# Optimization experiments

Hardware: AMD Instinct MI355X
Metric: run time of the kernel (lower is better)

The kernel has to match this reference:

```python
import jax, jax.numpy as jnp
import numpy as np

N, E, IN, H, O, ED = 20000, 100000, 167, 4, 256, 10
HID = H * O  # 1024
BN_EPS = 1e-5


def _bn(x, g, b):
    # BatchNorm1d in training mode: batch statistics over nodes
    mu = x.mean(0)
    var = x.var(0)
    return (x - mu) * jax.lax.rsqrt(var + BN_EPS) * g + b


def _gat(x, src, dst, ef, Wg, We, attn, at, cb, heads, out):
    # modified_GAT: multi-head attention with edge features + time scalar
    n = x.shape[0]
    h = (x @ Wg).reshape(n, heads, out)                 # [N,H,O]
    e = (ef[:, 1:] @ We).reshape(-1, heads, out)        # [E,H,O] edge-feature proj
    t = ef[:, 0]                                        # [E] time feature
    # node-level attention scores (avoids materializing [E,H,O] twice)
    s_src = jnp.einsum('nhd,hd->nh', h, attn[0])
    s_dst = jnp.einsum('nhd,hd->nh', h, attn[1])
    s_e = jnp.einsum('ehd,hd->eh', e, attn[2])
    logits = jax.nn.leaky_relu(s_src[src] + s_dst[dst] + s_e + t[:, None] * at, 0.2)  # [E,H]
    # attention normalization: softmax over incoming edges of each dst node
    m = jax.ops.segment_max(logits, dst, num_segments=n)
    m = jnp.where(jnp.isfinite(m), m, 0.0)
    p = jnp.exp(logits - m[dst])
    denom = jax.ops.segment_sum(p, dst, num_segments=n)
    w = p / (denom[dst] + 1e-16)                        # [E,H]
    msg = w[:, :, None] * (h[src] + e)                  # [E,H,O]
    agg = jax.ops.segment_sum(msg, dst, num_segments=n) # [N,H,O]
    return agg.reshape(n, heads * out) + cb


def setup_inputs() -> dict:
    key = jax.random.key(0)
    ks = iter(jax.random.split(key, 64))

    def nrm(shape, s):
        return jax.random.normal(next(ks), shape, dtype=jnp.float32) * np.float32(s)

    d = {}
    d['x'] = jax.random.normal(next(ks), (N, IN), dtype=jnp.float32)
    d['edge_index'] = jax.random.randint(next(ks), (2, E), 0, N)
    d['edge_attr'] = jax.random.uniform(next(ks), (E, ED + 2), dtype=jnp.float32)
    conv_dims = [(IN, H, O), (HID, H, O), (HID, 1, 2)]
    for i, (fin, hh, oo) in enumerate(conv_dims, 1):
        d[f'Wg{i}'] = nrm((fin, hh * oo), 1.0 / np.sqrt(fin))
        d[f'We{i}'] = nrm((ED, hh * oo), 1.0 / np.sqrt(ED))
        d[f'attn{i}'] = nrm((3, hh, oo), 0.1)
        d[f'at{i}'] = nrm((hh,), 0.1)
        d[f'cb{i}'] = jnp.zeros((hh * oo,), jnp.float32)
    lin_dims = [(IN, HID), (HID, HID), (HID, 2)]
    bn_dims = [IN, HID, HID]
    for i, (fin, fo) in enumerate(lin_dims, 1):
        d[f'lw{i}'] = nrm((fin, fo), 1.0 / np.sqrt(fin))
        d[f'lb{i}'] = jnp.zeros((fo,), jnp.float32)
        d[f'g{i}'] = jnp.ones((bn_dims[i - 1],), jnp.float32)
        d[f'b{i}'] = jnp.zeros((bn_dims[i - 1],), jnp.float32)
    return d


def reference(x, edge_index, edge_attr,
              Wg1, We1, attn1, at1, cb1, lw1, lb1, g1, b1,
              Wg2, We2, attn2, at2, cb2, lw2, lb2, g2, b2,
              Wg3, We3, attn3, at3, cb3, lw3, lb3, g3, b3):
    src, dst = edge_index[0], edge_index[1]
    ef = edge_attr[:, :-1]  # drop edge class column
    h = _bn(x, g1, b1)
    h = jax.nn.relu(h @ lw1 + lb1 + _gat(h, src, dst, ef, Wg1, We1, attn1, at1, cb1, H, O))
    h = _bn(h, g2, b2)
    h = jax.nn.relu(h @ lw2 + lb2 + _gat(h, src, dst, ef, Wg2, We2, attn2, at2, cb2, H, O))
    h = _bn(h, g3, b3)
    h = jax.nn.relu(h @ lw3 + lb3 + _gat(h, src, dst, ef, Wg3, We3, attn3, at3, cb3, 1, 2))
    return h
```

## Files before the change

kernel.cpp:

```cpp
#include <hip/hip_runtime.h>
#include <math.h>

#define NN 20000
#define EE 100000
#define FIN 167
#define KP1 256
#define HID 1024
#define OO 256
#define NB 16

typedef unsigned short u16;
typedef short bf16x8 __attribute__((ext_vector_type(8)));
typedef short s16x4  __attribute__((ext_vector_type(4)));
typedef float f32x4  __attribute__((ext_vector_type(4)));

__device__ __forceinline__ float bf(u16 u){ return __uint_as_float(((unsigned)u)<<16); }
__device__ __forceinline__ u16 fb(float v){
  unsigned u = __float_as_uint(v);
  return (u16)((u + 0x7FFFu + ((u>>16)&1u)) >> 16);
}
__device__ __forceinline__ float ldv(const float* p, long i){ return p[i]; }
__device__ __forceinline__ float ldv(const u16*   p, long i){ return bf(p[i]); }

__global__ void k_count(const int* __restrict__ ei, int* __restrict__ counts){
  int e = blockIdx.x*256 + threadIdx.x;
  if (e < EE) atomicAdd(&counts[ei[EE+e]], 1);
}

__global__ __launch_bounds__(256) void k_scan(const int* __restrict__ counts, int* __restrict__ iptr){
  __shared__ int sd[256];
  int tid = threadIdx.x;
  int carry = 0;
  for (int base=0; base<NN; base+=256){
    int i = base+tid;
    int v = (i<NN)? counts[i] : 0;
    sd[tid]=v;
    __syncthreads();
    for (int off=1; off<256; off<<=1){
      int t = (tid>=off)? sd[tid-off] : 0;
      __syncthreads();
      sd[tid] += t;
      __syncthreads();
    }
    if (i<NN) iptr[i] = carry + sd[tid] - v;
    carry += sd[255];
    __syncthreads();
  }
  if (tid==0) iptr[NN]=carry;
}

__global__ void k_fill(const int* __restrict__ ei, const int* __restrict__ iptr,
                       int* __restrict__ cursor, int* __restrict__ eid){
  int e = blockIdx.x*256 + threadIdx.x;
  if (e < EE){
    int d = ei[EE+e];
    int pos = atomicAdd(&cursor[d],1);
    eid[iptr[d]+pos] = e;
  }
}

template<typename T>
__global__ void k_bnstats(const T* __restrict__ X, float* __restrict__ sums, int F){
  int f = blockIdx.y*256 + threadIdx.x;
  if (f >= F) return;
  int r0 = blockIdx.x*100, r1 = r0+100;
  float s=0.f, s2=0.f;
  for (int r=r0;r<r1;r++){ float v = ldv(X,(long)r*F+f); s += v; s2 += v*v; }
  atomicAdd(&sums[f], s);
  atomicAdd(&sums[F+f], s2);
}

__global__ void k_bnfin(const float* __restrict__ sums, const float* __restrict__ g,
                        const float* __restrict__ b, float* __restrict__ scale,
                        float* __restrict__ shift, int F){
  int f = blockIdx.x*256 + threadIdx.x;
  if (f >= F) return;
  float mu  = sums[f]   * (1.f/NN);
  float var = sums[F+f] * (1.f/NN) - mu*mu;
  float sc  = rsqrtf(var + 1e-5f) * g[f];
  scale[f] = sc;
  shift[f] = b[f] - mu*sc;
}

__global__ __launch_bounds__(256) void k_foldT(const float* __restrict__ Wg, const float* __restrict__ Wl,
                        const float* __restrict__ scale,
                        u16* __restrict__ Wt, int K, int Kp){
  __shared__ float t[32][33];
  int k0 = blockIdx.x*32, c0 = blockIdx.y*32;
  int tx = threadIdx.x & 31, ty = threadIdx.x >> 5;
  bool second = (c0 >= HID);
  const float* W = second ? Wl : Wg;
  int cc0 = second ? c0 - HID : c0;
  #pragma unroll
  for (int i=0;i<4;i++){
    int k = k0 + ty + i*8;
    t[ty+i*8][tx] = (k < K) ? W[(long)k*HID + cc0 + tx] * scale[k] : 0.f;
  }
  __syncthreads();
  #pragma unroll
  for (int i=0;i<4;i++){
    int c = c0 + ty + i*8;
    Wt[(long)c*Kp + k0 + tx] = fb(t[tx][ty+i*8]);
  }
}

__global__ void k_cinit(const float* __restrict__ lb, float* __restrict__ cst){
  int c = blockIdx.x*256 + threadIdx.x;
  if (c < 2*HID) cst[c] = (c >= HID) ? lb[c-HID] : 0.f;
}

__global__ __launch_bounds__(256) void k_const(const float* __restrict__ Wg, const float* __restrict__ Wl,
                        const float* __restrict__ shift, float* __restrict__ cst, int K){
  int tx = threadIdx.x & 63, ty = threadIdx.x >> 6;
  int c = blockIdx.x*64 + tx;
  bool second = c >= HID;
  const float* W = second ? Wl : Wg;
  int cc = second ? c-HID : c;
  int k0 = blockIdx.y*128;
  int k1 = min(K, k0+128);
  float s = 0.f;
  for (int k=k0+ty; k<k1; k+=4) s += shift[k]*W[(long)k*HID+cc];
  __shared__ float red[256];
  red[threadIdx.x] = s;
  __syncthreads();
  if (ty == 0){
    float tot = red[tx] + red[tx+64] + red[tx+128] + red[tx+192];
    atomicAdd(&cst[c], tot);
  }
}

__global__ void k_cast(const float* __restrict__ x, u16* __restrict__ xb){
  long idx = (long)blockIdx.x*256 + threadIdx.x;
  if (idx >= (long)NN*KP1) return;
  int n = (int)(idx / KP1), k = (int)(idx % KP1);
  xb[idx] = (k<FIN)? fb(x[(long)n*FIN+k]) : (u16)0;
}

__global__ void k_we16(const float* __restrict__ We, u16* __restrict__ We16){
  int i = blockIdx.x*256 + threadIdx.x;
  if (i < 10*HID) We16[i] = fb(We[i]);
}

#define MF(a_,b_,c_) __builtin_amdgcn_mfma_f32_16x16x32_bf16(a_,b_,c_,0,0,0)
#define FENCE asm volatile("" ::: "memory")
#define BAR do { FENCE; __builtin_amdgcn_s_barrier(); FENCE; } while(0)

__global__ __launch_bounds__(512,2) void k_gemm(const u16* __restrict__ A, int K,
                     const u16* __restrict__ Wt, const float* __restrict__ cst,
                     u16* __restrict__ Chg, u16* __restrict__ Clin){
  __shared__ u16 lds[2][24576];
  int b = blockIdx.x;
  int wg = (b & 7)*158 + (b >> 3);
  int row0 = (wg >> 4)*256, col0 = (wg & 15)*128;
  int tid = threadIdx.x;
  int wave = tid >> 6, lane = tid & 63, quad = lane >> 4, lo = lane & 15;
  int wm = wave >> 1, wn = wave & 1;
  const u16* Apt[2];
  #pragma unroll
  for (int i=0;i<2;i++){
    int s = i*512 + tid, srow = s>>2;
    int gr = row0 + srow; if (gr >= NN) gr = NN-1;
    Apt[i] = A + (long)gr*K + (((s&3)^(srow&3))*8);
  }
  int brow = tid>>2;
  const u16* Bpt = Wt + (long)(col0 + brow)*K + ((((tid&3)^(brow&3)))*8);
  const char* ldsc = (const char*)&lds[0][0];
  int axor = lo & 3;
  int aoff = (wm*64 + lo)*64 + ((quad^axor)*16);
  int boff = 32768 + (wn*64 + lo)*64 + ((quad^axor)*16);
  int NT = K >> 6;
  f32x4 acc[4][4] = {};
  {
    u16* d = (u16*)&lds[0][0];
    __builtin_amdgcn_global_load_lds(Apt[0],      d +          tid*8, 16, 0, 0);
    __builtin_amdgcn_global_load_lds(Apt[1],      d +  4096 +  tid*8, 16, 0, 0);
    __builtin_amdgcn_global_load_lds(Bpt,         d + 16384 +  tid*8, 16, 0, 0);
    __builtin_amdgcn_global_load_lds(Apt[0] + 32, d +  8192 +  tid*8, 16, 0, 0);
    __builtin_amdgcn_global_load_lds(Apt[1] + 32, d + 12288 +  tid*8, 16, 0, 0);
    __builtin_amdgcn_global_load_lds(Bpt    + 32, d + 20480 +  tid*8, 16, 0, 0);
    asm volatile("s_waitcnt vmcnt(3)" ::: "memory");
    BAR;
  }
  for (int t=0; t<NT; t++){
    const char* Lb = ldsc + (t&1)*49152;
    u16* Sb = (u16*)&lds[0][0] + ((t&1)^1)*24576;
    int k0n = (t+1) << 6;
    int nx = (t+1 < NT);
    bf16x8 af[4], bfr[4];
    #pragma unroll
    for (int i=0;i<4;i++) af[i]  = *(const bf16x8*)(Lb + aoff + i*1024);
    #pragma unroll
    for (int n=0;n<4;n++) bfr[n] = *(const bf16x8*)(Lb + boff + n*1024);
    if (nx){
      __builtin_amdgcn_global_load_lds(Apt[0] + k0n, Sb +          tid*8, 16, 0, 0);
      __builtin_amdgcn_global_load_lds(Apt[1] + k0n, Sb +  4096 +  tid*8, 16, 0, 0);
      __builtin_amdgcn_global_load_lds(Bpt    + k0n, Sb + 16384 +  tid*8, 16, 0, 0);
    }
    #pragma unroll
    for (int i=0;i<4;i++)
      #pragma unroll
      for (int n=0;n<4;n++)
        acc[i][n] = MF(af[i], bfr[n], acc[i][n]);
    if (nx) asm volatile("s_waitcnt vmcnt(3)" ::: "memory");
    else    asm volatile("s_waitcnt vmcnt(0)" ::: "memory");
    BAR;
    #pragma unroll
    for (int i=0;i<4;i++) af[i]  = *(const bf16x8*)(Lb + 16384 + aoff + i*1024);
    #pragma unroll
    for (int n=0;n<4;n++) bfr[n] = *(const bf16x8*)(Lb +  8192 + boff + n*1024);
    if (nx){
      __builtin_amdgcn_global_load_lds(Apt[0] + k0n + 32, Sb +  8192 +  tid*8, 16, 0, 0);
      __builtin_amdgcn_global_load_lds(Apt[1] + k0n + 32, Sb + 12288 +  tid*8, 16, 0, 0);
      __builtin_amdgcn_global_load_lds(Bpt    + k0n + 32, Sb + 20480 +  tid*8, 16, 0, 0);
    }
    #pragma unroll
    for (int i=0;i<4;i++)
      #pragma unroll
      for (int n=0;n<4;n++)
        acc[i][n] = MF(af[i], bfr[n], acc[i][n]);
    if (nx) asm volatile("s_waitcnt vmcnt(3)" ::: "memory");
    BAR;
  }
  #pragma unroll
  for (int i=0;i<4;i++){
    #pragma unroll
    for (int n=0;n<4;n++){
      int col = col0 + wn*64 + n*16 + lo;
      float cs = cst[col];
      #pragma unroll
      for (int r=0;r<4;r++){
        int row = row0 + wm*64 + i*16 + quad*4 + r;
        if (row < NN){
          u16 o = fb(acc[i][n][r] + cs);
          if (col < HID) Chg[(long)row*HID + col] = o;
          else           Clin[(long)row*HID + col - HID] = o;
        }
      }
    }
  }
}
#undef MF
#undef BAR
#undef FENCE

__global__ __launch_bounds__(256) void k_sdot(const u16* __restrict__ hg, const float* __restrict__ attn,
                       float* __restrict__ ssrc, float* __restrict__ sdst){
  int unit = blockIdx.x*4 + (threadIdx.x >> 6);
  if (unit >= NN*4) return;
  int lane = threadIdx.x & 63;
  int n = unit >> 2, h = unit & 3;
  const u16* hp = hg + (long)n*HID + h*OO + lane*4;
  s16x4 v = *(const s16x4*)hp;
  float4 x0 = *(const float4*)(attn + h*OO + lane*4);
  float4 x1 = *(const float4*)(attn + HID + h*OO + lane*4);
  float f0 = bf((u16)v.x), f1 = bf((u16)v.y), f2 = bf((u16)v.z), f3 = bf((u16)v.w);
  float ss = f0*x0.x + f1*x0.y + f2*x0.z + f3*x0.w;
  float sd = f0*x1.x + f1*x1.y + f2*x1.z + f3*x1.w;
  #pragma unroll
  for (int off=32; off>0; off>>=1){
    ss += __shfl_down(ss, off);
    sd += __shfl_down(sd, off);
  }
  if (lane==0){ ssrc[unit]=ss; sdst[unit]=sd; }
}

__global__ void k_q(const float* __restrict__ We, const float* __restrict__ attn,
                    float* __restrict__ q){
  int t = threadIdx.x;
  if (t >= 40) return;
  int k = t >> 2, h = t & 3;
  float s = 0.f;
  for (int d=0; d<OO; d++) s += We[(long)k*HID + h*OO + d] * attn[2*HID + h*OO + d];
  q[k*4+h] = s;
}

__global__ void k_logits(const int* __restrict__ ei, const float* __restrict__ ea,
                         const float* __restrict__ q, const float* __restrict__ at,
                         const float* __restrict__ ssrc, const float* __restrict__ sdst,
                         float* __restrict__ L){
  int idx = blockIdx.x*256 + threadIdx.x;
  if (idx >= EE*4) return;
  int e = idx >> 2, h = idx & 3;
  int s = ei[e], dd = ei[EE+e];
  float se = 0.f;
  #pragma unroll
  for (int k=0;k<10;k++) se += ea[e*12+1+k] * q[k*4+h];
  float v = ssrc[s*4+h] + sdst[dd*4+h] + se + ea[e*12]*at[h];
  L[idx] = (v>0.f)? v : 0.2f*v;
}

__global__ void k_mden(const int* __restrict__ iptr, const int* __restrict__ eid,
                       const float* __restrict__ ea, float* __restrict__ L,
                       float* __restrict__ cw){
  int idx = blockIdx.x*256 + threadIdx.x;
  if (idx >= NN*4) return;
  int n = idx >> 2, h = idx & 3;
  int b = iptr[n], e1 = iptr[n+1];
  float mx = -INFINITY;
  for (int i=b;i<e1;i++) mx = fmaxf(mx, L[eid[i]*4+h]);
  if (b == e1) mx = 0.f;
  float s = 0.f;
  for (int i=b;i<e1;i++) s += expf(L[eid[i]*4+h] - mx);
  float dv = 1.f/(s + 1e-16f);
  float c[10] = {0.f,0.f,0.f,0.f,0.f,0.f,0.f,0.f,0.f,0.f};
  for (int i=b;i<e1;i++){
    int e = eid[i];
    float w = expf(L[e*4+h]-mx)*dv;
    L[e*4+h] = w;
    #pragma unroll
    for (int k=0;k<10;k++) c[k] += w*ea[e*12+1+k];
  }
  float* cp = cw + (long)idx*10;
  #pragma unroll
  for (int k=0;k<10;k++) cp[k] = c[k];
}

__global__ __launch_bounds__(256) void k_gath(
    const u16* __restrict__ hg, const int* __restrict__ ei,
    const int* __restrict__ iptr, const int* __restrict__ eid,
    const float* __restrict__ L,
    const float* __restrict__ cw,
    const u16* __restrict__ We16, const float* __restrict__ cb,
    u16* __restrict__ lio)
{
  __shared__ u16  sWe[10*HID];
  __shared__ float scb[HID];
  int tid = threadIdx.x;
  for (int i=tid;i<10*HID;i+=256) sWe[i] = We16[i];
  for (int i=tid;i<HID;i+=256) scb[i] = cb[i];
  __syncthreads();
  int d0 = blockIdx.x*NB, dend = min(NN, d0+NB);
  for (int d=d0; d<dend; d++){
    float acc[4];
    #pragma unroll
    for (int j=0;j<4;j++) acc[j] = bf(lio[(long)d*HID + tid + j*256]);
    int b0 = iptr[d], en = iptr[d+1];
    for (int i=b0;i<en;i++){
      int e = eid[i], s_ = ei[e];
      float4 w4 = *(const float4*)(L + (long)e*4);
      const u16* hgs = hg + (long)s_*HID + tid;
      acc[0] += w4.x*bf(hgs[0]);
      acc[1] += w4.y*bf(hgs[256]);
      acc[2] += w4.z*bf(hgs[512]);
      acc[3] += w4.w*bf(hgs[768]);
    }
    const float* cp = cw + (long)d*40;
    #pragma unroll
    for (int j=0;j<4;j++){
      float ew = 0.f;
      #pragma unroll
      for (int k=0;k<10;k++) ew += cp[j*10+k]*bf(sWe[k*HID + tid + j*256]);
      acc[j] += ew;
    }
    #pragma unroll
    for (int j=0;j<4;j++){
      int f = tid + j*256;
      lio[(long)d*HID+f] = fb(fmaxf(acc[j] + scb[f], 0.f));
    }
  }
}

__global__ __launch_bounds__(256) void k_n3(
    const u16* __restrict__ in, const float* __restrict__ scale, const float* __restrict__ shift,
    const float* __restrict__ Wg, const float* __restrict__ lw, const float* __restrict__ lb,
    const float* __restrict__ attn,
    float* __restrict__ hg3, float* __restrict__ lin3,
    float* __restrict__ ssrc, float* __restrict__ sdst)
{
  __shared__ float xin[1024];
  __shared__ float red[256];
  int n = blockIdx.x, tid = threadIdx.x;
  for (int k=tid;k<HID;k+=256) xin[k] = bf(in[(long)n*HID+k])*scale[k]+shift[k];
  __syncthreads();
  float p[4] = {0.f,0.f,0.f,0.f};
  for (int k=tid;k<HID;k+=256){
    float xv = xin[k];
    p[0] += xv*Wg[k*2];   p[1] += xv*Wg[k*2+1];
    p[2] += xv*lw[k*2];   p[3] += xv*lw[k*2+1];
  }
  float r[4];
  for (int q=0;q<4;q++){
    red[tid]=p[q]; __syncthreads();
    for (int o=128;o>0;o>>=1){ if(tid<o) red[tid]+=red[tid+o]; __syncthreads(); }
    r[q]=red[0]; __syncthreads();
  }
  if (tid==0){
    hg3[n*2]   = r[0];
    hg3[n*2+1] = r[1];
    lin3[n*2]   = r[2] + lb[0];
    lin3[n*2+1] = r[3] + lb[1];
    ssrc[n] = r[0]*attn[0] + r[1]*attn[1];
    sdst[n] = r[0]*attn[2] + r[1]*attn[3];
  }
}

__global__ void k_logits3(const int* __restrict__ ei, const float* __restrict__ ea,
                          const float* __restrict__ We, const float* __restrict__ attn,
                          const float* __restrict__ at, const float* __restrict__ ssrc,
                          const float* __restrict__ sdst, float* __restrict__ L){
  int e = blockIdx.x*256 + threadIdx.x;
  if (e >= EE) return;
  int s = ei[e], d = ei[EE+e];
  float e0=0.f, e1=0.f;
  #pragma unroll
  for (int k=0;k<10;k++){
    float c = ea[e*12+1+k];
    e0 += c*We[k*2]; e1 += c*We[k*2+1];
  }
  float se = e0*attn[4] + e1*attn[5];
  float v = ssrc[s] + sdst[d] + se + ea[e*12]*at[0];
  L[e] = (v>0.f)? v : 0.2f*v;
}

__global__ void k_mden3(const int* __restrict__ iptr, const int* __restrict__ eid,
                        const float* __restrict__ ea, float* __restrict__ L,
                        float* __restrict__ cw){
  int n = blockIdx.x*256 + threadIdx.x;
  if (n >= NN) return;
  int b = iptr[n], e1 = iptr[n+1];
  float mx = -INFINITY;
  for (int i=b;i<e1;i++) mx = fmaxf(mx, L[eid[i]]);
  if (b == e1) mx = 0.f;
  float s = 0.f;
  for (int i=b;i<e1;i++) s += expf(L[eid[i]] - mx);
  float dv = 1.f/(s+1e-16f);
  float c[10] = {0.f,0.f,0.f,0.f,0.f,0.f,0.f,0.f,0.f,0.f};
  for (int i=b;i<e1;i++){
    int e = eid[i];
    float w = expf(L[e]-mx)*dv;
    L[e] = w;
    #pragma unroll
    for (int k=0;k<10;k++) c[k] += w*ea[e*12+1+k];
  }
  float* cp = cw + (long)n*10;
  #pragma unroll
  for (int k=0;k<10;k++) cp[k] = c[k];
}

__global__ void k_gather3(const int* __restrict__ ei,
                          const int* __restrict__ iptr, const int* __restrict__ eid,
                          const float* __restrict__ L,
                          const float* __restrict__ cw,
                          const float* __restrict__ hg3,
                          const float* __restrict__ We, const float* __restrict__ lin3,
                          const float* __restrict__ cb, float* __restrict__ out){
  int n = blockIdx.x*256 + threadIdx.x;
  if (n >= NN) return;
  int b = iptr[n], en = iptr[n+1];
  const float* cp = cw + (long)n*10;
  float e0f=0.f, e1f=0.f;
  #pragma unroll
  for (int k=0;k<10;k++){ e0f += cp[k]*We[k*2]; e1f += cp[k]*We[k*2+1]; }
  float a0=0.f, a1=0.f;
  for (int i=b;i<en;i++){
    int e = eid[i], s_ = ei[e];
    float w = L[e];
    a0 += w*hg3[s_*2];
    a1 += w*hg3[s_*2+1];
  }
  out[n*2]   = fmaxf(lin3[n*2]  +a0+e0f+cb[0], 0.f);
  out[n*2+1] = fmaxf(lin3[n*2+1]+a1+e1f+cb[1], 0.f);
}

extern "C" void kernel_launch(void* const* d_in, const int* in_sizes, int n_in,
                              void* d_out, int out_size, void* d_ws, size_t ws_size,
                              hipStream_t stream){
  const int* ei = (const int*)d_in[1];

  long long sz[64];
  {
    const long long* s64 = (const long long*)(const void*)in_sizes;
    bool is64 = (n_in >= 2) && (in_sizes[0] == 3340000) && (in_sizes[1] == 0)
                && (s64[1] == 200000);
    for (int i=0;i<n_in && i<64;i++) sz[i] = is64 ? s64[i] : (long long)in_sizes[i];
  }

  int IWg[3], IWe[3], IAttn[3], IAt[3], ICb[3], ILw[3], ILb[3], IG[3], IB[3];
  if (n_in > 8 && sz[8] == (long long)HID*HID){
    for (int l=0;l<3;l++){
      IWg[l]=3+l*5; IWe[l]=4+l*5; IAttn[l]=5+l*5; IAt[l]=6+l*5; ICb[l]=7+l*5;
      ILw[l]=18+l*4; ILb[l]=19+l*4; IG[l]=20+l*4; IB[l]=21+l*4;
    }
  } else {
    int idx=3;
    for (int l=0;l<3;l++){
      IWg[l]=idx++; IWe[l]=idx++; IAttn[l]=idx++; IAt[l]=idx++; ICb[l]=idx++;
      ILw[l]=idx++; ILb[l]=idx++; IG[l]=idx++; IB[l]=idx++;
    }
  }
  #define FP(i) ((const float*)d_in[(i)])

  char* ws = (char*)d_ws;
  size_t off = 0;
  auto alloc = [&](size_t bytes)->void*{ void* p = ws + off; off += (bytes + 255) & ~(size_t)255; return p; };
  auto G = [](long n){ return (int)((n+255)/256); };

  u16*   buf0 = (u16*)  alloc((size_t)NN*HID*2);
  u16*   bufA = (u16*)  alloc((size_t)NN*HID*2);
  u16*   bufB = (u16*)  alloc((size_t)NN*HID*2);
  u16*   xbf  = (u16*)  alloc((size_t)NN*KP1*2);
  u16*   Wt   = (u16*)  alloc((size_t)2*HID*HID*2);
  u16*   We16 = (u16*)  alloc((size_t)10*HID*2);
  float* cst  = (float*)alloc(2*HID*4);
  float* L    = (float*)alloc((size_t)EE*4*4);
  float* m    = (float*)alloc((size_t)NN*4*4);
  float* dinv = (float*)alloc((size_t)NN*4*4);
  float* ssrc = (float*)alloc((size_t)NN*4*4);
  float* sdst = (float*)alloc((size_t)NN*4*4);
  int*   iptr = (int*)  alloc((size_t)(NN+4)*4);
  int*   cnts = (int*)  alloc((size_t)NN*4);
  int*   eid  = (int*)  alloc((size_t)EE*4);
  float* stats= (float*)alloc(2*HID*4);
  float* scale= (float*)alloc(HID*4);
  float* shift= (float*)alloc(HID*4);
  float* qbuf = (float*)alloc(64*4);
  float* hg3  = (float*)alloc((size_t)NN*2*4);
  float* lin3 = (float*)alloc((size_t)NN*2*4);
  float* cw   = (float*)alloc((size_t)NN*40*4);

  hipMemsetAsync(cnts, 0, NN*sizeof(int), stream);
  k_count<<<G(EE),256,0,stream>>>(ei, cnts);
  k_scan<<<1,256,0,stream>>>(cnts, iptr);
  hipMemsetAsync(cnts, 0, NN*sizeof(int), stream);
  k_fill<<<G(EE),256,0,stream>>>(ei, iptr, cnts, eid);

  int gg = 1264;
  int gsd = (NN*4+3)/4;

  {
    hipMemsetAsync(stats, 0, 2*FIN*sizeof(float), stream);
    dim3 bg(200, 1);
    k_bnstats<float><<<bg,256,0,stream>>>(FP(0), stats, FIN);
    k_bnfin<<<1,256,0,stream>>>(stats, FP(IG[0]), FP(IB[0]), scale, shift, FIN);
    k_cast<<<G((long)NN*KP1),256,0,stream>>>(FP(0), xbf);
    dim3 ft(KP1/32, 64);
    k_foldT<<<ft,256,0,stream>>>(FP(IWg[0]), FP(ILw[0]), scale, Wt, FIN, KP1);
    k_cinit<<<8,256,0,stream>>>(FP(ILb[0]), cst);
    dim3 cg(32, (FIN+127)/128);
    k_const<<<cg,256,0,stream>>>(FP(IWg[0]), FP(ILw[0]), shift, cst, FIN);
    k_we16<<<40,256,0,stream>>>(FP(IWe[0]), We16);
    k_gemm<<<gg,512,0,stream>>>(xbf, KP1, Wt, cst, buf0, bufA);
    k_sdot<<<gsd,256,0,stream>>>(buf0, FP(IAttn[0]), ssrc, sdst);
    k_q<<<1,64,0,stream>>>(FP(IWe[0]), FP(IAttn[0]), qbuf);
    k_logits<<<G(EE*4),256,0,stream>>>(ei, FP(2), qbuf, FP(IAt[0]), ssrc, sdst, L);
    k_mden<<<G(NN*4),256,0,stream>>>(iptr, eid, FP(2), L, cw);
    k_gath<<<(NN+NB-1)/NB,256,0,stream>>>(buf0, ei, iptr, eid, L, cw,
                                          We16, FP(ICb[0]), bufA);
  }
  {
    hipMemsetAsync(stats, 0, 2*HID*sizeof(float), stream);
    dim3 bg(200, 4);
    k_bnstats<u16><<<bg,256,0,stream>>>(bufA, stats, HID);
    k_bnfin<<<4,256,0,stream>>>(stats, FP(IG[1]), FP(IB[1]), scale, shift, HID);
    dim3 ft(HID/32, 64);
    k_foldT<<<ft,256,0,stream>>>(FP(IWg[1]), FP(ILw[1]), scale, Wt, HID, HID);
    k_cinit<<<8,256,0,stream>>>(FP(ILb[1]), cst);
    dim3 cg(32, HID/128);
    k_const<<<cg,256,0,stream>>>(FP(IWg[1]), FP(ILw[1]), shift, cst, HID);
    k_we16<<<40,256,0,stream>>>(FP(IWe[1]), We16);
    k_gemm<<<gg,512,0,stream>>>(bufA, HID, Wt, cst, buf0, bufB);
    k_sdot<<<gsd,256,0,stream>>>(buf0, FP(IAttn[1]), ssrc, sdst);
    k_q<<<1,64,0,stream>>>(FP(IWe[1]), FP(IAttn[1]), qbuf);
    k_logits<<<G(EE*4),256,0,stream>>>(ei, FP(2), qbuf, FP(IAt[1]), ssrc, sdst, L);
    k_mden<<<G(NN*4),256,0,stream>>>(iptr, eid, FP(2), L, cw);
    k_gath<<<(NN+NB-1)/NB,256,0,stream>>>(buf0, ei, iptr, eid, L, cw,
                                          We16, FP(ICb[1]), bufB);
  }

  hipMemsetAsync(stats, 0, 2*HID*sizeof(float), stream);
  dim3 bg3(200, 4);
  k_bnstats<u16><<<bg3,256,0,stream>>>(bufB, stats, HID);
  k_bnfin<<<4,256,0,stream>>>(stats, FP(IG[2]), FP(IB[2]), scale, shift, HID);
  k_n3<<<NN,256,0,stream>>>(bufB, scale, shift, FP(IWg[2]), FP(ILw[2]), FP(ILb[2]),
                            FP(IAttn[2]), hg3, lin3, ssrc, sdst);
  k_logits3<<<G(EE),256,0,stream>>>(ei, FP(2), FP(IWe[2]), FP(IAttn[2]), FP(IAt[2]), ssrc, sdst, L);
  k_mden3<<<G(NN),256,0,stream>>>(iptr, eid, FP(2), L, cw);
  k_gather3<<<G(NN),256,0,stream>>>(ei, iptr, eid, L, cw, hg3,
                                    FP(IWe[2]), lin3, FP(ICb[2]), (float*)d_out);
}
```

Measured before the change: 912.5 us.

## Vectorize BN stats, logits, softmax kernels and fold BN into layer-3 projection

Several memory-bound kernels are reworked. BN statistics now read 8 bf16 values per thread with a shared-memory reduction and far fewer atomics. Logits and the per-node softmax now handle all 4 heads per thread using float4 loads, so each edge's attributes and indices are loaded once. The layer-3 node projection folds the BN scale and shift into a small precomputed weight and constant, then processes 4 nodes per block with wavefront shuffle reductions instead of one node per block with repeated tree reductions. The cost is fewer threads in the softmax kernel (one per node) and more registers per thread for the 40 accumulators.

```diff
diff --git a/kernel.cpp b/kernel.cpp
--- a/kernel.cpp
+++ b/kernel.cpp
@@ -68,6 +68,34 @@
   for (int r=r0;r<r1;r++){ float v = ldv(X,(long)r*F+f); s += v; s2 += v*v; }
   atomicAdd(&sums[f], s);
   atomicAdd(&sums[F+f], s2);
+}
+
+__global__ __launch_bounds__(256) void k_bnstats8(const u16* __restrict__ X, float* __restrict__ sums){
+  int tid = threadIdx.x;
+  int f8 = (tid & 127)*8;
+  int rbase = blockIdx.x*500;
+  float s[8]={0,0,0,0,0,0,0,0}, s2[8]={0,0,0,0,0,0,0,0};
+  for (int r=rbase + (tid>>7); r<rbase+500; r+=2){
+    bf16x8 v = *(const bf16x8*)(X + (long)r*HID + f8);
+    #pragma unroll
+    for (int j=0;j<8;j++){ float x=bf((u16)v[j]); s[j]+=x; s2[j]+=x*x; }
+  }
+  __shared__ float red[256][8];
+  #pragma unroll
+  for (int j=0;j<8;j++) red[tid][j]=s[j];
+  __syncthreads();
+  if (tid<128){
+    #pragma unroll
+    for (int j=0;j<8;j++) atomicAdd(&sums[f8+j], red[tid][j]+red[tid+128][j]);
+  }
+  __syncthreads();
+  #pragma unroll
+  for (int j=0;j<8;j++) red[tid][j]=s2[j];
+  __syncthreads();
+  if (tid<128){
+    #pragma unroll
+    for (int j=0;j<8;j++) atomicAdd(&sums[HID+f8+j], red[tid][j]+red[tid+128][j]);
+  }
 }
 
 __global__ void k_bnfin(const float* __restrict__ sums, const float* __restrict__ g,
@@ -278,41 +306,68 @@
                          const float* __restrict__ q, const float* __restrict__ at,
                          const float* __restrict__ ssrc, const float* __restrict__ sdst,
                          float* __restrict__ L){
-  int idx = blockIdx.x*256 + threadIdx.x;
-  if (idx >= EE*4) return;
-  int e = idx >> 2, h = idx & 3;
+  int e = blockIdx.x*256 + threadIdx.x;
+  if (e >= EE) return;
   int s = ei[e], dd = ei[EE+e];
-  float se = 0.f;
-  #pragma unroll
-  for (int k=0;k<10;k++) se += ea[e*12+1+k] * q[k*4+h];
-  float v = ssrc[s*4+h] + sdst[dd*4+h] + se + ea[e*12]*at[h];
-  L[idx] = (v>0.f)? v : 0.2f*v;
+  float4 a0 = *(const float4*)(ea + (long)e*12);
+  float4 a1 = *(const float4*)(ea + (long)e*12 + 4);
+  float4 a2 = *(const float4*)(ea + (long)e*12 + 8);
+  float t = a0.x;
+  float cc[10] = {a0.y,a0.z,a0.w, a1.x,a1.y,a1.z,a1.w, a2.x,a2.y,a2.z};
+  float4 ss = *(const float4*)(ssrc + (long)s*4);
+  float4 sd = *(const float4*)(sdst + (long)dd*4);
+  float sv[4] = {ss.x+sd.x, ss.y+sd.y, ss.z+sd.z, ss.w+sd.w};
+  float4 out;
+  #pragma unroll
+  for (int h=0;h<4;h++){
+    float se = 0.f;
+    #pragma unroll
+    for (int k=0;k<10;k++) se += cc[k]*q[k*4+h];
+    float v = sv[h] + se + t*at[h];
+    ((float*)&out)[h] = (v>0.f)? v : 0.2f*v;
+  }
+  *(float4*)(L + (long)e*4) = out;
 }
 
 __global__ void k_mden(const int* __restrict__ iptr, const int* __restrict__ eid,
                        const float* __restrict__ ea, float* __restrict__ L,
                        float* __restrict__ cw){
-  int idx = blockIdx.x*256 + threadIdx.x;
-  if (idx >= NN*4) return;
-  int n = idx >> 2, h = idx & 3;
+  int n = blockIdx.x*256 + threadIdx.x;
+  if (n >= NN) return;
   int b = iptr[n], e1 = iptr[n+1];
-  float mx = -INFINITY;
-  for (int i=b;i<e1;i++) mx = fmaxf(mx, L[eid[i]*4+h]);
-  if (b == e1) mx = 0.f;
-  float s = 0.f;
-  for (int i=b;i<e1;i++) s += expf(L[eid[i]*4+h] - mx);
-  float dv = 1.f/(s + 1e-16f);
-  float c[10] = {0.f,0.f,0.f,0.f,0.f,0.f,0.f,0.f,0.f,0.f};
+  float m0=-INFINITY, m1=-INFINITY, m2=-INFINITY, m3=-INFINITY;
+  for (int i=b;i<e1;i++){
+    float4 l = *(const float4*)(L + (long)eid[i]*4);
+    m0=fmaxf(m0,l.x); m1=fmaxf(m1,l.y); m2=fmaxf(m2,l.z); m3=fmaxf(m3,l.w);
+  }
+  if (b==e1){ m0=m1=m2=m3=0.f; }
+  float s0=0.f,s1=0.f,s2=0.f,s3=0.f;
+  for (int i=b;i<e1;i++){
+    float4 l = *(const float4*)(L + (long)eid[i]*4);
+    s0+=expf(l.x-m0); s1+=expf(l.y-m1); s2+=expf(l.z-m2); s3+=expf(l.w-m3);
+  }
+  float d0=1.f/(s0+1e-16f), d1=1.f/(s1+1e-16f), d2=1.f/(s2+1e-16f), d3=1.f/(s3+1e-16f);
+  float c[4][10] = {};
   for (int i=b;i<e1;i++){
     int e = eid[i];
-    float w = expf(L[e*4+h]-mx)*dv;
-    L[e*4+h] = w;
-    #pragma unroll
-    for (int k=0;k<10;k++) c[k] += w*ea[e*12+1+k];
-  }
-  float* cp = cw + (long)idx*10;
-  #pragma unroll
-  for (int k=0;k<10;k++) cp[k] = c[k];
+    float4 l = *(const float4*)(L + (long)e*4);
+    float4 w = { expf(l.x-m0)*d0, expf(l.y-m1)*d1, expf(l.z-m2)*d2, expf(l.w-m3)*d3 };
+    *(float4*)(L + (long)e*4) = w;
+    float4 a0 = *(const float4*)(ea + (long)e*12);
+    float4 a1 = *(const float4*)(ea + (long)e*12 + 4);
+    float4 a2 = *(const float4*)(ea + (long)e*12 + 8);
+    float cc[10] = {a0.y,a0.z,a0.w, a1.x,a1.y,a1.z,a1.w, a2.x,a2.y,a2.z};
+    #pragma unroll
+    for (int k=0;k<10;k++){
+      c[0][k] += w.x*cc[k]; c[1][k] += w.y*cc[k];
+      c[2][k] += w.z*cc[k]; c[3][k] += w.w*cc[k];
+    }
+  }
+  float* cp = cw + (long)n*40;
+  #pragma unroll
+  for (int h=0;h<4;h++)
+    #pragma unroll
+    for (int k=0;k<10;k++) cp[h*10+k] = c[h][k];
 }
 
 __global__ __launch_bounds__(256) void k_gath(
@@ -360,37 +415,76 @@
   }
 }
 
-__global__ __launch_bounds__(256) void k_n3(
-    const u16* __restrict__ in, const float* __restrict__ scale, const float* __restrict__ shift,
-    const float* __restrict__ Wg, const float* __restrict__ lw, const float* __restrict__ lb,
+__global__ void k_c4init(const float* __restrict__ lb, float* __restrict__ c4){
+  if (threadIdx.x==0 && blockIdx.x==0){ c4[0]=0.f; c4[1]=0.f; c4[2]=lb[0]; c4[3]=lb[1]; }
+}
+
+__global__ __launch_bounds__(256) void k_fold3(const float* __restrict__ Wg, const float* __restrict__ lw,
+                        const float* __restrict__ scale, const float* __restrict__ shift,
+                        float* __restrict__ W4, float* __restrict__ c4){
+  int k = blockIdx.x*256 + threadIdx.x;
+  float sc = scale[k], sh = shift[k];
+  float w0=Wg[k*2], w1=Wg[k*2+1], l0=lw[k*2], l1=lw[k*2+1];
+  float4 o = {w0*sc, w1*sc, l0*sc, l1*sc};
+  *(float4*)(W4 + (long)k*4) = o;
+  __shared__ float red[256][4];
+  int tid = threadIdx.x;
+  red[tid][0]=sh*w0; red[tid][1]=sh*w1; red[tid][2]=sh*l0; red[tid][3]=sh*l1;
+  __syncthreads();
+  for (int o2=128;o2>0;o2>>=1){
+    if (tid<o2){
+      #pragma unroll
+      for (int j=0;j<4;j++) red[tid][j]+=red[tid+o2][j];
+    }
+    __syncthreads();
+  }
+  if (tid==0){
+    #pragma unroll
+    for (int j=0;j<4;j++) atomicAdd(&c4[j], red[0][j]);
+  }
+}
+
+__global__ __launch_bounds__(256) void k_n3(const u16* __restrict__ in,
+    const float* __restrict__ W4, const float* __restrict__ c4,
     const float* __restrict__ attn,
     float* __restrict__ hg3, float* __restrict__ lin3,
     float* __restrict__ ssrc, float* __restrict__ sdst)
 {
-  __shared__ float xin[1024];
-  __shared__ float red[256];
-  int n = blockIdx.x, tid = threadIdx.x;
-  for (int k=tid;k<HID;k+=256) xin[k] = bf(in[(long)n*HID+k])*scale[k]+shift[k];
-  __syncthreads();
-  float p[4] = {0.f,0.f,0.f,0.f};
-  for (int k=tid;k<HID;k+=256){
-    float xv = xin[k];
-    p[0] += xv*Wg[k*2];   p[1] += xv*Wg[k*2+1];
-    p[2] += xv*lw[k*2];   p[3] += xv*lw[k*2+1];
-  }
-  float r[4];
-  for (int q=0;q<4;q++){
-    red[tid]=p[q]; __syncthreads();
-    for (int o=128;o>0;o>>=1){ if(tid<o) red[tid]+=red[tid+o]; __syncthreads(); }
-    r[q]=red[0]; __syncthreads();
-  }
-  if (tid==0){
-    hg3[n*2]   = r[0];
-    hg3[n*2+1] = r[1];
-    lin3[n*2]   = r[2] + lb[0];
-    lin3[n*2+1] = r[3] + lb[1];
-    ssrc[n] = r[0]*attn[0] + r[1]*attn[1];
-    sdst[n] = r[0]*attn[2] + r[1]*attn[3];
+  __shared__ float sW[HID*4];
+  __shared__ float sx[4][HID];
+  int tid = threadIdx.x;
+  int n0 = blockIdx.x*4;
+  for (int i=tid; i<HID; i+=256) *(float4*)&sW[i*4] = *(const float4*)(W4 + (long)i*4);
+  for (int idx=tid; idx<512; idx+=256){
+    int rr = idx>>7, ch = idx&127;
+    bf16x8 v = *(const bf16x8*)(in + (long)(n0+rr)*HID + ch*8);
+    #pragma unroll
+    for (int j=0;j<8;j++) sx[rr][ch*8+j] = bf((u16)v[j]);
+  }
+  __syncthreads();
+  int w = tid>>6, lane = tid&63;
+  float p0=0.f,p1=0.f,p2=0.f,p3=0.f;
+  #pragma unroll
+  for (int g=0; g<16; g++){
+    int k = g*64 + lane;
+    float x = sx[w][k];
+    float4 wv = *(const float4*)&sW[k*4];
+    p0 += x*wv.x; p1 += x*wv.y; p2 += x*wv.z; p3 += x*wv.w;
+  }
+  #pragma unroll
+  for (int off=32; off>0; off>>=1){
+    p0 += __shfl_down(p0, off);
+    p1 += __shfl_down(p1, off);
+    p2 += __shfl_down(p2, off);
+    p3 += __shfl_down(p3, off);
+  }
+  if (lane==0){
+    int n = n0 + w;
+    float r0=p0+c4[0], r1=p1+c4[1], r2=p2+c4[2], r3=p3+c4[3];
+    hg3[n*2]=r0; hg3[n*2+1]=r1;
+    lin3[n*2]=r2; lin3[n*2+1]=r3;
+    ssrc[n]=r0*attn[0]+r1*attn[1];
+    sdst[n]=r0*attn[2]+r1*attn[3];
   }
 }
 
@@ -503,8 +597,6 @@
   u16*   We16 = (u16*)  alloc((size_t)10*HID*2);
   float* cst  = (float*)alloc(2*HID*4);
   float* L    = (float*)alloc((size_t)EE*4*4);
-  float* m    = (float*)alloc((size_t)NN*4*4);
-  float* dinv = (float*)alloc((size_t)NN*4*4);
   float* ssrc = (float*)alloc((size_t)NN*4*4);
   float* sdst = (float*)alloc((size_t)NN*4*4);
   int*   iptr = (int*)  alloc((size_t)(NN+4)*4);
@@ -517,6 +609,8 @@
   float* hg3  = (float*)alloc((size_t)NN*2*4);
   float* lin3 = (float*)alloc((size_t)NN*2*4);
   float* cw   = (float*)alloc((size_t)NN*40*4);
+  float* W4   = (float*)alloc((size_t)HID*4*4);
+  float* c4   = (float*)alloc(4*4);
 
   hipMemsetAsync(cnts, 0, NN*sizeof(int), stream);
   k_count<<<G(EE),256,0,stream>>>(ei, cnts);
@@ -542,15 +636,14 @@
     k_gemm<<<gg,512,0,stream>>>(xbf, KP1, Wt, cst, buf0, bufA);
     k_sdot<<<gsd,256,0,stream>>>(buf0, FP(IAttn[0]), ssrc, sdst);
     k_q<<<1,64,0,stream>>>(FP(IWe[0]), FP(IAttn[0]), qbuf);
-    k_logits<<<G(EE*4),256,0,stream>>>(ei, FP(2), qbuf, FP(IAt[0]), ssrc, sdst, L);
-    k_mden<<<G(NN*4),256,0,stream>>>(iptr, eid, FP(2), L, cw);
+    k_logits<<<G(EE),256,0,stream>>>(ei, FP(2), qbuf, FP(IAt[0]), ssrc, sdst, L);
+    k_mden<<<G(NN),256,0,stream>>>(iptr, eid, FP(2), L, cw);
     k_gath<<<(NN+NB-1)/NB,256,0,stream>>>(buf0, ei, iptr, eid, L, cw,
                                           We16, FP(ICb[0]), bufA);
   }
   {
     hipMemsetAsync(stats, 0, 2*HID*sizeof(float), stream);
-    dim3 bg(200, 4);
-    k_bnstats<u16><<<bg,256,0,stream>>>(bufA, stats, HID);
+    k_bnstats8<<<40,256,0,stream>>>(bufA, stats);
     k_bnfin<<<4,256,0,stream>>>(stats, FP(IG[1]), FP(IB[1]), scale, shift, HID);
     dim3 ft(HID/32, 64);
     k_foldT<<<ft,256,0,stream>>>(FP(IWg[1]), FP(ILw[1]), scale, Wt, HID, HID);
@@ -561,18 +654,18 @@
     k_gemm<<<gg,512,0,stream>>>(bufA, HID, Wt, cst, buf0, bufB);
     k_sdot<<<gsd,256,0,stream>>>(buf0, FP(IAttn[1]), ssrc, sdst);
     k_q<<<1,64,0,stream>>>(FP(IWe[1]), FP(IAttn[1]), qbuf);
-    k_logits<<<G(EE*4),256,0,stream>>>(ei, FP(2), qbuf, FP(IAt[1]), ssrc, sdst, L);
-    k_mden<<<G(NN*4),256,0,stream>>>(iptr, eid, FP(2), L, cw);
+    k_logits<<<G(EE),256,0,stream>>>(ei, FP(2), qbuf, FP(IAt[1]), ssrc, sdst, L);
+    k_mden<<<G(NN),256,0,stream>>>(iptr, eid, FP(2), L, cw);
     k_gath<<<(NN+NB-1)/NB,256,0,stream>>>(buf0, ei, iptr, eid, L, cw,
                                           We16, FP(ICb[1]), bufB);
   }
 
   hipMemsetAsync(stats, 0, 2*HID*sizeof(float), stream);
-  dim3 bg3(200, 4);
-  k_bnstats<u16><<<bg3,256,0,stream>>>(bufB, stats, HID);
+  k_bnstats8<<<40,256,0,stream>>>(bufB, stats);
   k_bnfin<<<4,256,0,stream>>>(stats, FP(IG[2]), FP(IB[2]), scale, shift, HID);
-  k_n3<<<NN,256,0,stream>>>(bufB, scale, shift, FP(IWg[2]), FP(ILw[2]), FP(ILb[2]),
-                            FP(IAttn[2]), hg3, lin3, ssrc, sdst);
+  k_c4init<<<1,64,0,stream>>>(FP(ILb[2]), c4);
+  k_fold3<<<HID/256,256,0,stream>>>(FP(IWg[2]), FP(ILw[2]), scale, shift, W4, c4);
+  k_n3<<<NN/4,256,0,stream>>>(bufB, W4, c4, FP(IAttn[2]), hg3, lin3, ssrc, sdst);
   k_logits3<<<G(EE),256,0,stream>>>(ei, FP(2), FP(IWe[2]), FP(IAttn[2]), FP(IAt[2]), ssrc, sdst, L);
   k_mden3<<<G(NN),256,0,stream>>>(iptr, eid, FP(2), L, cw);
   k_gather3<<<G(NN),256,0,stream>>>(ei, iptr, eid, L, cw, hg3,
```

Result: slower. 1.002 ms (+9.8%).
